# Performance work log

Measured on AMD Instinct MI355X. Metric: run time of the kernel, lower is better.

Reference implementation:

```python
import jax, jax.numpy as jnp
import numpy as np


def setup_inputs() -> dict:
    key = jax.random.key(0)
    ks = jax.random.split(key, 7)
    B, C, H, W = 16, 256, 1, 4096
    x = jax.random.normal(ks[0], (B, C, H, W), dtype=jnp.float32)
    init = lambda k, s: jax.random.normal(k, s, dtype=jnp.float32) * 0.02
    return {
        "x": x,
        "Wq": init(ks[1], (C, C)), "bq": jnp.zeros((C,), jnp.float32),
        "Wk": init(ks[2], (C, C)), "bk": jnp.zeros((C,), jnp.float32),
        "Wv": init(ks[3], (C, C)), "bv": jnp.zeros((C,), jnp.float32),
    }


def reference(x, Wq, bq, Wk, bk, Wv, bv):
    B, C, H, W = x.shape
    xs = jnp.transpose(x[:, :, 0, :], (0, 2, 1))  # [B, W, C]
    Q = xs @ Wq.T + bq  # [B, W, C]
    K = xs @ Wk.T + bk
    V = xs @ Wv.T + bv
    scale = jnp.sqrt(jnp.asarray(C, dtype=Q.dtype))

    # radius-1 sliding window along width; pad so window gather is static
    Kp = jnp.pad(K, ((0, 0), (1, 1), (0, 0)))  # [B, W+2, C]
    Vp = jnp.pad(V, ((0, 0), (1, 1), (0, 0)))
    idx = jnp.arange(W)[:, None] + jnp.arange(3)[None, :]  # padded indices [W,3]
    pos = idx - 1  # original positions (may be -1 or W -> invalid at edges)
    valid = (pos >= 0) & (pos < W)  # [W, 3]

    Kw = Kp[:, idx]  # [B, W, 3, C]
    Vw = Vp[:, idx]  # [B, W, 3, C]

    scores = jnp.einsum('bwc,bwkc->bwk', Q, Kw) / scale  # [B, W, 3]
    scores = jnp.where(valid[None], scores, jnp.asarray(-1e9, scores.dtype))
    attn = jax.nn.softmax(scores, axis=-1)
    out = jnp.einsum('bwk,bwkc->bwc', attn, Vw)  # [B, W, C]
    # [B, W, C] -> [B, C, 1, W]
    return jnp.transpose(out, (0, 2, 1))[:, :, None, :]
```

## Files before the change

kernel.cpp:

```cpp
#include <hip/hip_runtime.h>
#include <hip/hip_bf16.h>

#define C_DIM 256
#define W_DIM 4096
#define WI 62
#define NCH 67
#define LDS_BYTES 39424

typedef unsigned short u16;
typedef short s16x8 __attribute__((ext_vector_type(8)));
typedef unsigned short u16x8 __attribute__((ext_vector_type(8)));
typedef unsigned short u16x4 __attribute__((ext_vector_type(4)));
typedef float f32x16 __attribute__((ext_vector_type(16)));

__device__ __forceinline__ u16 f2b(float f) {
  return __builtin_bit_cast(u16, __float2bfloat16(f));
}
__device__ __forceinline__ float b2f(u16 u) {
  return __builtin_bit_cast(float, ((unsigned)u) << 16);
}

__global__ __launch_bounds__(256) void prep_kernel(
    const float* __restrict__ Wq, const float* __restrict__ bq,
    const float* __restrict__ Wk, const float* __restrict__ bk,
    const float* __restrict__ Wv, char* __restrict__ ws) {
  u16* Mb   = (u16*)ws;
  u16* Wvb  = (u16*)(ws + 131072);
  float* u0 = (float*)(ws + 262144);
  float* u1 = (float*)(ws + 263168);
  float* c0p = (float*)(ws + 264192);
  int bid = blockIdx.x, t = threadIdx.x;
  if (bid < 256) {
    __shared__ float Wqs[256*17];
    __shared__ float Wks[256*17];
    int i0 = (bid >> 4) << 4, j0 = (bid & 15) << 4;
    for (int it = 0; it < 16; ++it) {
      int e = t + 256*it; int a = e >> 4, ii = e & 15;
      Wqs[a*17+ii] = Wq[a*256 + i0 + ii];
      Wks[a*17+ii] = Wk[a*256 + j0 + ii];
    }
    __syncthreads();
    int ii = t >> 4, jj = t & 15;
    float acc = 0.f;
    #pragma unroll 8
    for (int a = 0; a < 256; ++a) acc += Wqs[a*17+ii] * Wks[a*17+jj];
    Mb[(i0+ii)*256 + j0 + jj] = f2b(acc);
  } else if (bid == 256) {
    int j = t;
    float a0 = 0.f, a1 = 0.f;
    #pragma unroll 4
    for (int a = 0; a < 256; ++a) {
      a0 += bq[a] * Wk[a*256 + j];
      a1 += bk[a] * Wq[a*256 + j];
    }
    u0[j] = a0; u1[j] = a1;
    __shared__ float red[256];
    red[t] = bq[t] * bk[t];
    __syncthreads();
    if (t == 0) { float s = 0.f; for (int a = 0; a < 256; ++a) s += red[a]; *c0p = s; }
  } else {
    int base = ((bid - 257)*256 + t) * 4;
    const float4 v = *reinterpret_cast<const float4*>(Wv + base);
    ushort4 pk = make_ushort4(f2b(v.x), f2b(v.y), f2b(v.z), f2b(v.w));
    *reinterpret_cast<ushort4*>(Wvb + base) = pk;
  }
}

__global__ __launch_bounds__(512, 6) void main_kernel(
    const float* __restrict__ x, const char* __restrict__ ws,
    const float* __restrict__ bv, float* __restrict__ out) {
  const u16* Mb   = (const u16*)ws;
  const u16* Wvb  = (const u16*)(ws + 131072);
  const float* u0 = (const float*)(ws + 262144);
  const float* u1 = (const float*)(ws + 263168);
  const float c0  = *(const float*)(ws + 264192);

  extern __shared__ char lds[];
  u16* Xt    = (u16*)lds;
  float* Ps  = (float*)(lds + 32768);
  float* ABs = (float*)(lds + 38912);

  const int bid = blockIdx.x;
  const int t = threadIdx.x;
  const int wv = t >> 6, l = t & 63;
  const int col = l & 31, half = l >> 5;

  const int b  = bid / NCH;
  const int cw = bid % NCH;
  const int w0 = cw * WI;
  const float* xb = x + (size_t)b * (C_DIM*W_DIM);
  float* outb = out + (size_t)b * (C_DIM*W_DIM);

  {
    int wg = w0 - 1 + l;
    bool ok = (wg >= 0) && (wg < W_DIM);
    const float* xp = xb + wg;
    float xr[32];
    #pragma unroll
    for (int r = 0; r < 4; ++r)
      #pragma unroll
      for (int e = 0; e < 8; ++e)
        xr[r*8+e] = ok ? xp[(size_t)((wv + 8*r)*8 + e) * W_DIM] : 0.f;

    float pa = 0.f, pb_ = 0.f;
    #pragma unroll
    for (int r = 0; r < 4; ++r) {
      int kk = wv + 8*r;
      union { u16 u[8]; u16x8 vv; } pk;
      #pragma unroll
      for (int e = 0; e < 8; ++e) {
        float v = xr[r*8+e];
        pk.u[e] = f2b(v);
        int c = kk*8 + e;
        pa  += u0[c] * v;
        pb_ += u1[c] * v;
      }
      *reinterpret_cast<u16x8*>(Xt + (kk*64 + l)*8) = pk.vv;
    }
    Ps[wv*64 + l] = pa;
    Ps[512 + wv*64 + l] = pb_;
  }
  __syncthreads();

  f32x16 acc0, acc1;
  #pragma unroll
  for (int r = 0; r < 16; ++r) { acc0[r] = 0.f; acc1[r] = 0.f; }
  {
    const u16* Arow = Mb + (32*wv + col)*256 + 8*half;
    #pragma unroll
    for (int kk = 0; kk < 16; ++kk) {
      s16x8 a = *reinterpret_cast<const s16x8*>(Arow + 16*kk);
      const u16* Bb = Xt + (2*kk + half)*64*8;
      s16x8 b0 = *reinterpret_cast<const s16x8*>(Bb + col*8);
      s16x8 b1 = *reinterpret_cast<const s16x8*>(Bb + (col+32)*8);
      acc0 = __builtin_amdgcn_mfma_f32_32x32x16_bf16(a, b0, acc0, 0, 0, 0);
      acc1 = __builtin_amdgcn_mfma_f32_32x32x16_bf16(a, b1, acc1, 0, 0, 0);
    }
  }
  if (t < 128) {
    int which = t >> 6, jj = t & 63;
    float s = 0.f;
    #pragma unroll
    for (int g = 0; g < 8; ++g) s += Ps[which*512 + g*64 + jj];
    ABs[which*64 + jj] = s;
  }
  __syncthreads();

  {
    float t0s0=0.f,t0s1=0.f,t0s2=0.f,t1s0=0.f,t1s1=0.f,t1s2=0.f;
    const int e0 = 4*half;
    int jm0 = (col > 0) ? col-1 : 0;
    int jp1 = (col < 31) ? col+33 : 63;
    #pragma unroll
    for (int q = 0; q < 4; ++q) {
      const u16* base = Xt + (4*wv + q)*64*8 + e0;
      u16x4 xT0m = *reinterpret_cast<const u16x4*>(base + jm0*8);
      u16x4 xT0c = *reinterpret_cast<const u16x4*>(base + col*8);
      u16x4 xT0p = *reinterpret_cast<const u16x4*>(base + (col+1)*8);
      u16x4 xT1m = *reinterpret_cast<const u16x4*>(base + (col+31)*8);
      u16x4 xT1c = *reinterpret_cast<const u16x4*>(base + (col+32)*8);
      u16x4 xT1p = *reinterpret_cast<const u16x4*>(base + jp1*8);
      #pragma unroll
      for (int r4 = 0; r4 < 4; ++r4) {
        float g0 = acc0[4*q+r4], g1 = acc1[4*q+r4];
        t0s1 += g0 * b2f(xT0c[r4]);
        t0s0 += g0 * b2f(xT0p[r4]);
        t0s2 += g0 * b2f(xT0m[r4]);
        t1s1 += g1 * b2f(xT1c[r4]);
        t1s0 += g1 * b2f(xT1p[r4]);
        t1s2 += g1 * b2f(xT1m[r4]);
      }
    }
    t0s0 += __shfl_xor(t0s0, 32); t0s1 += __shfl_xor(t0s1, 32);
    t0s2 += __shfl_xor(t0s2, 32); t1s0 += __shfl_xor(t1s0, 32);
    t1s1 += __shfl_xor(t1s1, 32); t1s2 += __shfl_xor(t1s2, 32);
    float* PBw = Ps + wv*64;
    if (half == 0) {
      PBw[0*512 + col+1]  = t0s0;
      PBw[1*512 + col]    = t0s1;
      if (col >= 1) PBw[2*512 + col-1] = t0s2;
      if (col < 31) PBw[0*512 + col+33] = t1s0;
      PBw[1*512 + col+32] = t1s1;
      PBw[2*512 + col+31] = t1s2;
    }
  }
  __syncthreads();

  {
    int lp2 = (l < 62) ? l+2 : 63;
    float d0 = 0.f, d1 = 0.f, d2 = 0.f;
    #pragma unroll
    for (int g = 0; g < 8; ++g) {
      d0 += Ps[0*512 + g*64 + l+1 - ((l==63)?1:0)];
      d1 += Ps[1*512 + g*64 + l+1 - ((l==63)?1:0)];
      d2 += Ps[2*512 + g*64 + ((l>=62)?62:l+1)];
    }
    float am = ABs[l], ac = ABs[(l<63)?l+1:63], ap = ABs[lp2];
    float be = ABs[64 + ((l<63)?l+1:63)];
    float sc0 = (d0 + am + be + c0) * 0.0625f;
    float sc1 = (d1 + ac + be + c0) * 0.0625f;
    float sc2 = (d2 + ap + be + c0) * 0.0625f;
    int w = w0 + l;
    bool v0 = (w >= 1), v2 = (w + 1 < W_DIM);
    const float NEG = -1e30f;
    float m = fmaxf(v0 ? sc0 : NEG, fmaxf(sc1, v2 ? sc2 : NEG));
    float e0v = v0 ? __expf(sc0 - m) : 0.f;
    float e1v = __expf(sc1 - m);
    float e2v = v2 ? __expf(sc2 - m) : 0.f;
    float inv = 1.f / (e0v + e1v + e2v);
    float a0 = e0v*inv, a1 = e1v*inv, a2 = e2v*inv;
    const bool wr = (l <= 61);
    #pragma unroll
    for (int kg = 0; kg < 4; ++kg) {
      int kk = 4*wv + kg;
      u16* base = Xt + kk*64*8;
      u16x8 xm  = *reinterpret_cast<const u16x8*>(base + l*8);
      u16x8 xc_ = *reinterpret_cast<const u16x8*>(base + ((l<63)?l+1:63)*8);
      u16x8 xp  = *reinterpret_cast<const u16x8*>(base + lp2*8);
      union { u16 u[8]; u16x8 vv; } pk;
      #pragma unroll
      for (int e = 0; e < 8; ++e)
        pk.u[e] = f2b(a0*b2f(xm[e]) + a1*b2f(xc_[e]) + a2*b2f(xp[e]));
      if (wr) *reinterpret_cast<u16x8*>(base + (l+1)*8) = pk.vv;
    }
  }
  __syncthreads();

  {
    #pragma unroll
    for (int r = 0; r < 16; ++r) { acc0[r] = 0.f; acc1[r] = 0.f; }
    const u16* Arow2 = Wvb + (32*wv + col)*256 + 8*half;
    #pragma unroll
    for (int kk = 0; kk < 16; ++kk) {
      s16x8 a = *reinterpret_cast<const s16x8*>(Arow2 + 16*kk);
      const u16* Bb = Xt + (2*kk + half)*64*8;
      s16x8 b0 = *reinterpret_cast<const s16x8*>(Bb + (1+col)*8);
      s16x8 b1 = *reinterpret_cast<const s16x8*>(Bb + (((col<31)?(33+col):63))*8);
      acc0 = __builtin_amdgcn_mfma_f32_32x32x16_bf16(a, b0, acc0, 0, 0, 0);
      acc1 = __builtin_amdgcn_mfma_f32_32x32x16_bf16(a, b1, acc1, 0, 0, 0);
    }
    float bvr[16];
    #pragma unroll
    for (int q = 0; q < 4; ++q) {
      float4 t4 = *reinterpret_cast<const float4*>(bv + 32*wv + 8*q + 4*half);
      bvr[4*q+0] = t4.x; bvr[4*q+1] = t4.y; bvr[4*q+2] = t4.z; bvr[4*q+3] = t4.w;
    }
    int wg0 = w0 + col;
    int wg1 = w0 + 32 + col;
    bool st0 = (wg0 < W_DIM);
    bool st1 = (col <= 29) && (wg1 < W_DIM);
    #pragma unroll
    for (int r = 0; r < 16; ++r) {
      int crow = 32*wv + (r&3) + 8*(r>>2) + 4*half;
      if (st0) outb[(size_t)crow*W_DIM + wg0] = acc0[r] + bvr[r];
      if (st1) outb[(size_t)crow*W_DIM + wg1] = acc1[r] + bvr[r];
    }
  }
}

extern "C" void kernel_launch(void* const* d_in, const int* in_sizes, int n_in,
                              void* d_out, int out_size, void* d_ws, size_t ws_size,
                              hipStream_t stream) {
  (void)in_sizes; (void)n_in; (void)out_size; (void)ws_size;
  const float* x  = (const float*)d_in[0];
  const float* Wq = (const float*)d_in[1];
  const float* bq = (const float*)d_in[2];
  const float* Wk = (const float*)d_in[3];
  const float* bk = (const float*)d_in[4];
  const float* Wv = (const float*)d_in[5];
  const float* bv = (const float*)d_in[6];
  float* out = (float*)d_out;
  char* ws = (char*)d_ws;

  hipFuncSetAttribute((const void*)main_kernel,
                      hipFuncAttributeMaxDynamicSharedMemorySize, LDS_BYTES);
  prep_kernel<<<321, 256, 0, stream>>>(Wq, bq, Wk, bk, Wv, ws);
  main_kernel<<<16 * NCH, 512, LDS_BYTES, stream>>>(x, ws, bv, out);
}
```

Measured before the change: 89.99 us.

## Halve width tile to 32 columns for smaller LDS and higher occupancy

Shrinks each block's width tile from 64 columns (62 interior) to 32 columns (30 interior), so each wave runs one MFMA accumulator instead of two. Block count roughly doubles, LDS use per block halves, and launch bounds rise to 8 blocks per CU. The aim is more parallelism and better latency hiding. In exchange the halo overhead grows from 2/64 to 2/32, the Mb/Wv weight rows are reloaded per block twice as often, and the 30-column output stores are less coalesced.

```diff
diff --git a/kernel.cpp b/kernel.cpp
--- a/kernel.cpp
+++ b/kernel.cpp
@@ -3,9 +3,9 @@
 
 #define C_DIM 256
 #define W_DIM 4096
-#define WI 62
-#define NCH 67
-#define LDS_BYTES 39424
+#define WI 30
+#define NCH 137
+#define LDS_BYTES 20736
 
 typedef unsigned short u16;
 typedef short s16x8 __attribute__((ext_vector_type(8)));
@@ -66,7 +66,7 @@
   }
 }
 
-__global__ __launch_bounds__(512, 6) void main_kernel(
+__global__ __launch_bounds__(512, 8) void main_kernel(
     const float* __restrict__ x, const char* __restrict__ ws,
     const float* __restrict__ bv, float* __restrict__ out) {
   const u16* Mb   = (const u16*)ws;
@@ -77,13 +77,14 @@
 
   extern __shared__ char lds[];
   u16* Xt    = (u16*)lds;
-  float* Ps  = (float*)(lds + 32768);
-  float* ABs = (float*)(lds + 38912);
+  float* Ps  = (float*)(lds + 16384);
+  float* ABs = (float*)(lds + 20480);
 
   const int bid = blockIdx.x;
   const int t = threadIdx.x;
   const int wv = t >> 6, l = t & 63;
   const int col = l & 31, half = l >> 5;
+  const int idx16 = 2*wv + half;
 
   const int b  = bid / NCH;
   const int cw = bid % NCH;
@@ -92,115 +93,103 @@
   float* outb = out + (size_t)b * (C_DIM*W_DIM);
 
   {
-    int wg = w0 - 1 + l;
+    int wg = w0 - 1 + col;
     bool ok = (wg >= 0) && (wg < W_DIM);
     const float* xp = xb + wg;
-    float xr[32];
-    #pragma unroll
-    for (int r = 0; r < 4; ++r)
+    float xr[16];
+    #pragma unroll
+    for (int g = 0; g < 2; ++g)
       #pragma unroll
       for (int e = 0; e < 8; ++e)
-        xr[r*8+e] = ok ? xp[(size_t)((wv + 8*r)*8 + e) * W_DIM] : 0.f;
+        xr[g*8+e] = ok ? xp[(size_t)((idx16*2+g)*8 + e) * W_DIM] : 0.f;
 
     float pa = 0.f, pb_ = 0.f;
     #pragma unroll
-    for (int r = 0; r < 4; ++r) {
-      int kk = wv + 8*r;
+    for (int g = 0; g < 2; ++g) {
+      int kk = idx16*2 + g;
       union { u16 u[8]; u16x8 vv; } pk;
       #pragma unroll
       for (int e = 0; e < 8; ++e) {
-        float v = xr[r*8+e];
+        float v = xr[g*8+e];
         pk.u[e] = f2b(v);
         int c = kk*8 + e;
         pa  += u0[c] * v;
         pb_ += u1[c] * v;
       }
-      *reinterpret_cast<u16x8*>(Xt + (kk*64 + l)*8) = pk.vv;
-    }
-    Ps[wv*64 + l] = pa;
-    Ps[512 + wv*64 + l] = pb_;
-  }
-  __syncthreads();
-
-  f32x16 acc0, acc1;
+      *reinterpret_cast<u16x8*>(Xt + (kk*32 + col)*8) = pk.vv;
+    }
+    Ps[idx16*32 + col] = pa;
+    Ps[512 + idx16*32 + col] = pb_;
+  }
+  __syncthreads();
+
+  f32x16 acc;
   #pragma unroll
-  for (int r = 0; r < 16; ++r) { acc0[r] = 0.f; acc1[r] = 0.f; }
+  for (int r = 0; r < 16; ++r) acc[r] = 0.f;
   {
     const u16* Arow = Mb + (32*wv + col)*256 + 8*half;
     #pragma unroll
     for (int kk = 0; kk < 16; ++kk) {
       s16x8 a = *reinterpret_cast<const s16x8*>(Arow + 16*kk);
-      const u16* Bb = Xt + (2*kk + half)*64*8;
-      s16x8 b0 = *reinterpret_cast<const s16x8*>(Bb + col*8);
-      s16x8 b1 = *reinterpret_cast<const s16x8*>(Bb + (col+32)*8);
-      acc0 = __builtin_amdgcn_mfma_f32_32x32x16_bf16(a, b0, acc0, 0, 0, 0);
-      acc1 = __builtin_amdgcn_mfma_f32_32x32x16_bf16(a, b1, acc1, 0, 0, 0);
-    }
-  }
-  if (t < 128) {
-    int which = t >> 6, jj = t & 63;
+      s16x8 b0 = *reinterpret_cast<const s16x8*>(Xt + ((2*kk + half)*32 + col)*8);
+      acc = __builtin_amdgcn_mfma_f32_32x32x16_bf16(a, b0, acc, 0, 0, 0);
+    }
+  }
+  if (t < 64) {
+    int which = t >> 5, jj = t & 31;
     float s = 0.f;
     #pragma unroll
-    for (int g = 0; g < 8; ++g) s += Ps[which*512 + g*64 + jj];
-    ABs[which*64 + jj] = s;
-  }
-  __syncthreads();
-
-  {
-    float t0s0=0.f,t0s1=0.f,t0s2=0.f,t1s0=0.f,t1s1=0.f,t1s2=0.f;
+    for (int g = 0; g < 16; ++g) s += Ps[which*512 + g*32 + jj];
+    ABs[which*32 + jj] = s;
+  }
+  __syncthreads();
+
+  {
+    float s0 = 0.f, s1 = 0.f, s2 = 0.f;
     const int e0 = 4*half;
-    int jm0 = (col > 0) ? col-1 : 0;
-    int jp1 = (col < 31) ? col+33 : 63;
+    int jm = (col > 0)  ? col-1 : 0;
+    int jp = (col < 31) ? col+1 : 31;
     #pragma unroll
     for (int q = 0; q < 4; ++q) {
-      const u16* base = Xt + (4*wv + q)*64*8 + e0;
-      u16x4 xT0m = *reinterpret_cast<const u16x4*>(base + jm0*8);
-      u16x4 xT0c = *reinterpret_cast<const u16x4*>(base + col*8);
-      u16x4 xT0p = *reinterpret_cast<const u16x4*>(base + (col+1)*8);
-      u16x4 xT1m = *reinterpret_cast<const u16x4*>(base + (col+31)*8);
-      u16x4 xT1c = *reinterpret_cast<const u16x4*>(base + (col+32)*8);
-      u16x4 xT1p = *reinterpret_cast<const u16x4*>(base + jp1*8);
+      const u16* base = Xt + (4*wv + q)*32*8 + e0;
+      u16x4 xm = *reinterpret_cast<const u16x4*>(base + jm*8);
+      u16x4 xc = *reinterpret_cast<const u16x4*>(base + col*8);
+      u16x4 xp = *reinterpret_cast<const u16x4*>(base + jp*8);
       #pragma unroll
       for (int r4 = 0; r4 < 4; ++r4) {
-        float g0 = acc0[4*q+r4], g1 = acc1[4*q+r4];
-        t0s1 += g0 * b2f(xT0c[r4]);
-        t0s0 += g0 * b2f(xT0p[r4]);
-        t0s2 += g0 * b2f(xT0m[r4]);
-        t1s1 += g1 * b2f(xT1c[r4]);
-        t1s0 += g1 * b2f(xT1p[r4]);
-        t1s2 += g1 * b2f(xT1m[r4]);
+        float g0 = acc[4*q + r4];
+        s2 += g0 * b2f(xm[r4]);
+        s1 += g0 * b2f(xc[r4]);
+        s0 += g0 * b2f(xp[r4]);
       }
     }
-    t0s0 += __shfl_xor(t0s0, 32); t0s1 += __shfl_xor(t0s1, 32);
-    t0s2 += __shfl_xor(t0s2, 32); t1s0 += __shfl_xor(t1s0, 32);
-    t1s1 += __shfl_xor(t1s1, 32); t1s2 += __shfl_xor(t1s2, 32);
-    float* PBw = Ps + wv*64;
+    s0 += __shfl_xor(s0, 32);
+    s1 += __shfl_xor(s1, 32);
+    s2 += __shfl_xor(s2, 32);
     if (half == 0) {
-      PBw[0*512 + col+1]  = t0s0;
-      PBw[1*512 + col]    = t0s1;
-      if (col >= 1) PBw[2*512 + col-1] = t0s2;
-      if (col < 31) PBw[0*512 + col+33] = t1s0;
-      PBw[1*512 + col+32] = t1s1;
-      PBw[2*512 + col+31] = t1s2;
-    }
-  }
-  __syncthreads();
-
-  {
-    int lp2 = (l < 62) ? l+2 : 63;
+      float* PBw = Ps + wv*32;
+      if (col < 31) PBw[0*256 + col+1] = s0;
+      PBw[1*256 + col] = s1;
+      if (col >= 1)  PBw[2*256 + col-1] = s2;
+    }
+  }
+  __syncthreads();
+
+  {
+    int jr = (col <= 29) ? col+1 : 30;
     float d0 = 0.f, d1 = 0.f, d2 = 0.f;
     #pragma unroll
     for (int g = 0; g < 8; ++g) {
-      d0 += Ps[0*512 + g*64 + l+1 - ((l==63)?1:0)];
-      d1 += Ps[1*512 + g*64 + l+1 - ((l==63)?1:0)];
-      d2 += Ps[2*512 + g*64 + ((l>=62)?62:l+1)];
-    }
-    float am = ABs[l], ac = ABs[(l<63)?l+1:63], ap = ABs[lp2];
-    float be = ABs[64 + ((l<63)?l+1:63)];
+      d0 += Ps[0*256 + g*32 + jr];
+      d1 += Ps[1*256 + g*32 + jr];
+      d2 += Ps[2*256 + g*32 + jr];
+    }
+    float am = ABs[jr-1], ac = ABs[jr], ap = ABs[jr+1];
+    float be = ABs[32 + jr];
     float sc0 = (d0 + am + be + c0) * 0.0625f;
     float sc1 = (d1 + ac + be + c0) * 0.0625f;
     float sc2 = (d2 + ap + be + c0) * 0.0625f;
-    int w = w0 + l;
+    int w = w0 + col;
     bool v0 = (w >= 1), v2 = (w + 1 < W_DIM);
     const float NEG = -1e30f;
     float m = fmaxf(v0 ? sc0 : NEG, fmaxf(sc1, v2 ? sc2 : NEG));
@@ -209,35 +198,33 @@
     float e2v = v2 ? __expf(sc2 - m) : 0.f;
     float inv = 1.f / (e0v + e1v + e2v);
     float a0 = e0v*inv, a1 = e1v*inv, a2 = e2v*inv;
-    const bool wr = (l <= 61);
-    #pragma unroll
-    for (int kg = 0; kg < 4; ++kg) {
-      int kk = 4*wv + kg;
-      u16* base = Xt + kk*64*8;
-      u16x8 xm  = *reinterpret_cast<const u16x8*>(base + l*8);
-      u16x8 xc_ = *reinterpret_cast<const u16x8*>(base + ((l<63)?l+1:63)*8);
-      u16x8 xp  = *reinterpret_cast<const u16x8*>(base + lp2*8);
+    const bool wr = (col <= 29);
+    #pragma unroll
+    for (int g = 0; g < 2; ++g) {
+      int kk = idx16*2 + g;
+      u16* base = Xt + kk*32*8;
+      u16x8 xm  = *reinterpret_cast<const u16x8*>(base + ((col<=29)?col:29)*8);
+      u16x8 xc_ = *reinterpret_cast<const u16x8*>(base + jr*8);
+      u16x8 xp  = *reinterpret_cast<const u16x8*>(base + (jr+1)*8);
       union { u16 u[8]; u16x8 vv; } pk;
       #pragma unroll
       for (int e = 0; e < 8; ++e)
         pk.u[e] = f2b(a0*b2f(xm[e]) + a1*b2f(xc_[e]) + a2*b2f(xp[e]));
-      if (wr) *reinterpret_cast<u16x8*>(base + (l+1)*8) = pk.vv;
-    }
-  }
-  __syncthreads();
-
-  {
-    #pragma unroll
-    for (int r = 0; r < 16; ++r) { acc0[r] = 0.f; acc1[r] = 0.f; }
+      if (wr) *reinterpret_cast<u16x8*>(base + (col+1)*8) = pk.vv;
+    }
+  }
+  __syncthreads();
+
+  {
+    #pragma unroll
+    for (int r = 0; r < 16; ++r) acc[r] = 0.f;
     const u16* Arow2 = Wvb + (32*wv + col)*256 + 8*half;
+    int jB = (col < 31) ? col+1 : 31;
     #pragma unroll
     for (int kk = 0; kk < 16; ++kk) {
       s16x8 a = *reinterpret_cast<const s16x8*>(Arow2 + 16*kk);
-      const u16* Bb = Xt + (2*kk + half)*64*8;
-      s16x8 b0 = *reinterpret_cast<const s16x8*>(Bb + (1+col)*8);
-      s16x8 b1 = *reinterpret_cast<const s16x8*>(Bb + (((col<31)?(33+col):63))*8);
-      acc0 = __builtin_amdgcn_mfma_f32_32x32x16_bf16(a, b0, acc0, 0, 0, 0);
-      acc1 = __builtin_amdgcn_mfma_f32_32x32x16_bf16(a, b1, acc1, 0, 0, 0);
+      s16x8 b0 = *reinterpret_cast<const s16x8*>(Xt + ((2*kk + half)*32 + jB)*8);
+      acc = __builtin_amdgcn_mfma_f32_32x32x16_bf16(a, b0, acc, 0, 0, 0);
     }
     float bvr[16];
     #pragma unroll
@@ -245,15 +232,12 @@
       float4 t4 = *reinterpret_cast<const float4*>(bv + 32*wv + 8*q + 4*half);
       bvr[4*q+0] = t4.x; bvr[4*q+1] = t4.y; bvr[4*q+2] = t4.z; bvr[4*q+3] = t4.w;
     }
-    int wg0 = w0 + col;
-    int wg1 = w0 + 32 + col;
-    bool st0 = (wg0 < W_DIM);
-    bool st1 = (col <= 29) && (wg1 < W_DIM);
+    int wgo = w0 + col;
+    bool st = (col <= 29) && (wgo < W_DIM);
     #pragma unroll
     for (int r = 0; r < 16; ++r) {
       int crow = 32*wv + (r&3) + 8*(r>>2) + 4*half;
-      if (st0) outb[(size_t)crow*W_DIM + wg0] = acc0[r] + bvr[r];
-      if (st1) outb[(size_t)crow*W_DIM + wg1] = acc1[r] + bvr[r];
+      if (st) outb[(size_t)crow*W_DIM + wgo] = acc[r] + bvr[r];
     }
   }
 }
```

After: 119.9 us. 33.3% more time.
